# Performance work log

Measured on AMD Instinct MI355X. Metric: run time of the kernel, lower is better.

The kernel has to match this reference:

```python
import jax, jax.numpy as jnp
import numpy as np

N_NODES = 20000
N_EDGES = 320000
IN_CH = 256
HID = 128
HEADS = 4
OUT_CH = 200
NUM_GRAPHS = 64
NEG_SLOPE = 0.2


def setup_inputs() -> dict:
    key = jax.random.key(0)
    ks = jax.random.split(key, 16)
    x = jax.random.normal(ks[0], (N_NODES, IN_CH), dtype=jnp.float32)
    edge_index = jax.random.randint(ks[1], (2, N_EDGES), 0, N_NODES, dtype=jnp.int64)
    batch = jnp.sort(jax.random.randint(ks[2], (N_NODES,), 0, NUM_GRAPHS, dtype=jnp.int64))

    def lin(k, fan_in, fan_out):
        return jax.random.normal(k, (fan_in, fan_out), dtype=jnp.float32) / np.sqrt(fan_in)

    def att(k, h, c):
        return jax.random.normal(k, (h, c), dtype=jnp.float32) / np.sqrt(c)

    return {
        "x": x, "edge_index": edge_index, "batch": batch,
        "W1": lin(ks[3], IN_CH, HEADS * HID),
        "a_src1": att(ks[4], HEADS, HID), "a_dst1": att(ks[5], HEADS, HID),
        "b1": jnp.zeros((HEADS * HID,), jnp.float32),
        "W2": lin(ks[6], HEADS * HID, HEADS * HID),
        "a_src2": att(ks[7], HEADS, HID), "a_dst2": att(ks[8], HEADS, HID),
        "b2": jnp.zeros((HEADS * HID,), jnp.float32),
        "W3": lin(ks[9], HEADS * HID, HID),
        "a_src3": att(ks[10], 1, HID), "a_dst3": att(ks[11], 1, HID),
        "b3": jnp.zeros((HID,), jnp.float32),
        "fc_w": lin(ks[12], HID, OUT_CH),
        "fc_b": jnp.zeros((OUT_CH,), jnp.float32),
    }


def gat_conv(x, src, dst, W, a_src, a_dst, bias):
    """PyG GATConv (concat=True, negative_slope=0.2, self-loops appended by caller)."""
    N = x.shape[0]
    heads, out_ch = a_src.shape
    h = (x @ W).reshape(N, heads, out_ch)                 # [N,H,C]
    alpha_s = jnp.einsum('nhc,hc->nh', h, a_src)          # [N,H]
    alpha_d = jnp.einsum('nhc,hc->nh', h, a_dst)
    e = jax.nn.leaky_relu(alpha_s[src] + alpha_d[dst], NEG_SLOPE)  # [E,H]
    # segment softmax over edges sharing the same target node
    m = jax.ops.segment_max(e, dst, num_segments=N)
    e = jnp.exp(e - m[dst])
    denom = jax.ops.segment_sum(e, dst, num_segments=N)
    alpha = e / (denom[dst] + 1e-16)                      # [E,H]
    msg = h[src] * alpha[:, :, None]                      # [E,H,C]
    out = jax.ops.segment_sum(msg, dst, num_segments=N)   # [N,H,C]
    return out.reshape(N, heads * out_ch) + bias


def reference(x, edge_index, batch, W1, a_src1, a_dst1, b1,
              W2, a_src2, a_dst2, b2, W3, a_src3, a_dst3, b3, fc_w, fc_b):
    N = x.shape[0]
    loop = jnp.arange(N, dtype=edge_index.dtype)
    src = jnp.concatenate([edge_index[0], loop])
    dst = jnp.concatenate([edge_index[1], loop])

    h = jax.nn.elu(gat_conv(x, src, dst, W1, a_src1, a_dst1, b1))
    h = jax.nn.elu(gat_conv(h, src, dst, W2, a_src2, a_dst2, b2))
    h = jax.nn.elu(gat_conv(h, src, dst, W3, a_src3, a_dst3, b3))

    # global_mean_pool over graph ids
    sums = jax.ops.segment_sum(h, batch, num_segments=NUM_GRAPHS)
    cnts = jax.ops.segment_sum(jnp.ones((N,), h.dtype), batch, num_segments=NUM_GRAPHS)
    pooled = sums / jnp.maximum(cnts, 1.0)[:, None]       # [G,HID]
    # F.dropout with training=False is identity
    logits = pooled @ fc_w + fc_b                          # [G,OUT_CH]
    return logits
```

## Files before the change

kernel.cpp:

```cpp
#include <hip/hip_runtime.h>
#include <hip/hip_bf16.h>
#include <stdint.h>

#define N_NODES   20000
#define N_EDGES   320000
#define E_TOT     (N_EDGES + N_NODES)
#define IN_CH     256
#define HID       128
#define HEADS     4
#define OUT_CH    200
#define NUM_GRAPHS 64
#define M_PAD     20096

typedef __bf16 bf16_t;
typedef __bf16 bf16x8 __attribute__((ext_vector_type(8)));
typedef __bf16 bf16x2 __attribute__((ext_vector_type(2)));
typedef float  f32x4  __attribute__((ext_vector_type(4)));

__device__ __forceinline__ bool detect_bf16(const unsigned short* __restrict__ xu16) {
  int lane = threadIdx.x & 63;
  unsigned short v = xu16[2 * lane];
  int e = (v >> 7) & 0xff;
  unsigned long long b = __ballot(e >= 90 && e <= 160);
  return __popcll(b) >= 40;
}
__device__ __forceinline__ bool detect_i64(const unsigned* __restrict__ eidx) {
  int lane = threadIdx.x & 63;
  unsigned long long b = __ballot(eidx[2 * lane + 1] == 0u);
  return __popcll(b) >= 32;
}

struct SmallCvt {
  const void* src[11];
  bf16_t* dst[11];
  int n[11];
};

__global__ void prep(const void* __restrict__ W1, const void* __restrict__ W2,
                     const void* __restrict__ W3, bf16_t* __restrict__ W1T,
                     bf16_t* __restrict__ W2T, bf16_t* __restrict__ W3T,
                     SmallCvt tab, const unsigned short* __restrict__ xu16,
                     const int* __restrict__ eidx, const int* __restrict__ batch,
                     int* __restrict__ esrc, int* __restrict__ edst,
                     int* __restrict__ b32, int* __restrict__ deg) {
  bool isbf = detect_bf16(xu16);
  bool i64  = detect_i64((const unsigned*)eidx);
  int i = blockIdx.x * 256 + threadIdx.x;
  if (i < N_EDGES) {
    int s = i64 ? eidx[2 * i] : eidx[i];
    int d = i64 ? eidx[2 * (N_EDGES + i)] : eidx[N_EDGES + i];
    esrc[i] = s;
    edst[i] = d;
    atomicAdd(&deg[d], 1);
  }
  if (i < N_NODES) {
    b32[i] = i64 ? batch[2 * i] : batch[i];
    atomicAdd(&deg[i], 1);
  }
  if (i < 131072) {
    int k = i >> 9, nn = i & 511;
    bf16_t v = isbf ? ((const bf16_t*)W1)[i] : (bf16_t)((const float*)W1)[i];
    W1T[(size_t)nn * 256 + k] = v;
  } else if (i < 131072 + 262144) {
    int i2 = i - 131072;
    int k = i2 >> 9, nn = i2 & 511;
    bf16_t v = isbf ? ((const bf16_t*)W2)[i2] : (bf16_t)((const float*)W2)[i2];
    W2T[(size_t)nn * 512 + k] = v;
  } else if (i < 131072 + 262144 + 65536) {
    int i3 = i - 131072 - 262144;
    int k = i3 >> 7, nn = i3 & 127;
    bf16_t v = isbf ? ((const bf16_t*)W3)[i3] : (bf16_t)((const float*)W3)[i3];
    W3T[(size_t)nn * 512 + k] = v;
  } else {
    int j = i - 458752;
    for (int s = 0; s < 11; ++s) {
      if (j < tab.n[s]) {
        tab.dst[s][j] = isbf ? ((const bf16_t*)tab.src[s])[j]
                             : (bf16_t)((const float*)tab.src[s])[j];
        break;
      }
      j -= tab.n[s];
    }
  }
}

__launch_bounds__(1024)
__global__ void scan_deg_block(const int* __restrict__ deg, int* __restrict__ off,
                               int* __restrict__ cursor) {
  const int PT = 20;
  int t = threadIdx.x;
  int lane = t & 63, wid = t >> 6;
  int base = t * PT;
  int v[PT];
  int s = 0;
#pragma unroll
  for (int j = 0; j < PT; ++j) {
    int i = base + j;
    v[j] = (i < N_NODES) ? deg[i] : 0;
    s += v[j];
  }
  int x = s;
  for (int d = 1; d < 64; d <<= 1) {
    int y = __shfl_up(x, d);
    if (lane >= d) x += y;
  }
  __shared__ int wsum[16];
  if (lane == 63) wsum[wid] = x;
  __syncthreads();
  if (t < 16) {
    int y = wsum[t];
    for (int d = 1; d < 16; d <<= 1) {
      int z = __shfl_up(y, d);
      if (t >= d) y += z;
    }
    wsum[t] = y;
  }
  __syncthreads();
  int run = (wid > 0 ? wsum[wid - 1] : 0) + (x - s);
#pragma unroll
  for (int j = 0; j < PT; ++j) {
    int i = base + j;
    if (i < N_NODES) { off[i] = run; cursor[i] = 0; run += v[j]; }
  }
  if (t == 1023) off[N_NODES] = run;
}

__global__ void scatter_kernel(const int* __restrict__ esrc, const int* __restrict__ edst,
                               const int* __restrict__ off, int* __restrict__ cursor,
                               int* __restrict__ csr_src) {
  int e = blockIdx.x * 256 + threadIdx.x;
  if (e >= E_TOT) return;
  int s, d;
  if (e < N_EDGES) { s = esrc[e]; d = edst[e]; } else { s = d = e - N_EDGES; }
  int pos = off[d] + atomicAdd(&cursor[d], 1);
  csr_src[pos] = s;
}

template<bool MAYBE_F32, int NBN>
__launch_bounds__(256)
__global__ void gemm_bf16(const void* __restrict__ Av, const bf16_t* __restrict__ BT,
                          bf16_t* __restrict__ C, int M, int N, int K,
                          const bf16_t* __restrict__ a_src, const bf16_t* __restrict__ a_dst,
                          float* __restrict__ as, float* __restrict__ ad, int H) {
  bool isbf = MAYBE_F32 ? detect_bf16((const unsigned short*)Av) : true;
  const bf16_t* A  = (const bf16_t*)Av;
  const float*  Af = (const float*)Av;
  __shared__ bf16_t As[2][128 * 32];
  __shared__ bf16_t Bs[2][128 * 32];
  __shared__ float sred[2][128];
  __shared__ float dred[2][128];
  const int tid  = threadIdx.x;
  const int lane = tid & 63;
  const int w    = tid >> 6;
  const int wm   = w & 1, wn = w >> 1;
  const int id   = blockIdx.x;
  const int bmq  = id / (8 * NBN);
  const int rem  = id % (8 * NBN);
  const int bm   = (bmq * 8 + (rem & 7)) * 128;
  const int bn   = (rem >> 3) * 128;
  const int quad = lane >> 4;
  const int l16  = lane & 15;
  const int hd   = bn >> 7;

  f32x4 zero = {0.f, 0.f, 0.f, 0.f};
  f32x4 acc[4][4];
  for (int i = 0; i < 4; ++i)
    for (int j = 0; j < 4; ++j) acc[i][j] = zero;

  const int c0 = tid, c1 = tid + 256;
  const int r0 = c0 >> 2, s0 = c0 & 3;
  const int r1 = c1 >> 2, s1 = c1 & 3;
  int ga0 = bm + r0; if (ga0 > M - 1) ga0 = M - 1;
  int ga1 = bm + r1; if (ga1 > M - 1) ga1 = M - 1;

  auto stage = [&](int b, int k0) {
    __builtin_amdgcn_global_load_lds(
        (const __attribute__((address_space(1))) void*)(A + (size_t)ga0 * K + k0 + s0 * 8),
        (__attribute__((address_space(3))) void*)(&As[b][(size_t)(w * 64) * 8]), 16, 0, 0);
    __builtin_amdgcn_global_load_lds(
        (const __attribute__((address_space(1))) void*)(BT + (size_t)(bn + r0) * K + k0 + s0 * 8),
        (__attribute__((address_space(3))) void*)(&Bs[b][(size_t)(w * 64) * 8]), 16, 0, 0);
    __builtin_amdgcn_global_load_lds(
        (const __attribute__((address_space(1))) void*)(A + (size_t)ga1 * K + k0 + s1 * 8),
        (__attribute__((address_space(3))) void*)(&As[b][(size_t)(256 + w * 64) * 8]), 16, 0, 0);
    __builtin_amdgcn_global_load_lds(
        (const __attribute__((address_space(1))) void*)(BT + (size_t)(bn + r1) * K + k0 + s1 * 8),
        (__attribute__((address_space(3))) void*)(&Bs[b][(size_t)(256 + w * 64) * 8]), 16, 0, 0);
  };

  auto mma_step = [&](int b) {
    bf16x8 af[4], bfr[4];
    for (int mt = 0; mt < 4; ++mt) {
      int m_local = wm * 64 + mt * 16 + l16;
      af[mt] = *(const bf16x8*)(&As[b][m_local * 32 + quad * 8]);
    }
    for (int nt = 0; nt < 4; ++nt) {
      int n_local = wn * 64 + nt * 16 + l16;
      bfr[nt] = *(const bf16x8*)(&Bs[b][n_local * 32 + quad * 8]);
    }
    for (int mt = 0; mt < 4; ++mt)
      for (int nt = 0; nt < 4; ++nt)
        acc[mt][nt] = __builtin_amdgcn_mfma_f32_16x16x32_bf16(af[mt], bfr[nt], acc[mt][nt], 0, 0, 0);
  };

  if (!MAYBE_F32 || isbf) {
    stage(0, 0);
    __syncthreads();
    const int NT = K >> 5;
    for (int t = 0; t < NT; ++t) {
      int cur = t & 1;
      if (t + 1 < NT) stage(cur ^ 1, (t + 1) << 5);
      mma_step(cur);
      __syncthreads();
    }
  } else {
    for (int k0 = 0; k0 < K; k0 += 32) {
      bf16x8 va0, va1;
      const float* p0 = Af + (size_t)ga0 * K + k0 + s0 * 8;
      const float* p1 = Af + (size_t)ga1 * K + k0 + s1 * 8;
      f32x4 l0 = *(const f32x4*)p0, h0 = *(const f32x4*)(p0 + 4);
      f32x4 l1 = *(const f32x4*)p1, h1 = *(const f32x4*)(p1 + 4);
      for (int j = 0; j < 4; ++j) {
        va0[j] = (bf16_t)l0[j]; va0[j + 4] = (bf16_t)h0[j];
        va1[j] = (bf16_t)l1[j]; va1[j + 4] = (bf16_t)h1[j];
      }
      bf16x8 vb0 = *(const bf16x8*)(BT + (size_t)(bn + r0) * K + k0 + s0 * 8);
      bf16x8 vb1 = *(const bf16x8*)(BT + (size_t)(bn + r1) * K + k0 + s1 * 8);
      __syncthreads();
      *(bf16x8*)(&As[0][c0 * 8]) = va0;
      *(bf16x8*)(&Bs[0][c0 * 8]) = vb0;
      *(bf16x8*)(&As[0][c1 * 8]) = va1;
      *(bf16x8*)(&Bs[0][c1 * 8]) = vb1;
      __syncthreads();
      mma_step(0);
    }
  }

  for (int mt = 0; mt < 4; ++mt) {
    for (int r = 0; r < 4; ++r) {
      int m = bm + wm * 64 + mt * 16 + quad * 4 + r;
      if (m >= M) continue;
      for (int nt = 0; nt < 4; ++nt) {
        int n = bn + wn * 64 + nt * 16 + l16;
        C[(size_t)m * N + n] = (bf16_t)acc[mt][nt][r];
      }
    }
  }

  float av[4], dv[4];
  for (int nt = 0; nt < 4; ++nt) {
    int ch = wn * 64 + nt * 16 + l16;
    av[nt] = (float)a_src[hd * 128 + ch];
    dv[nt] = (float)a_dst[hd * 128 + ch];
  }
  for (int mt = 0; mt < 4; ++mt) {
    for (int r = 0; r < 4; ++r) {
      float s = acc[mt][0][r] * av[0] + acc[mt][1][r] * av[1]
              + acc[mt][2][r] * av[2] + acc[mt][3][r] * av[3];
      float d = acc[mt][0][r] * dv[0] + acc[mt][1][r] * dv[1]
              + acc[mt][2][r] * dv[2] + acc[mt][3][r] * dv[3];
      for (int o = 1; o < 16; o <<= 1) {
        s += __shfl_xor(s, o);
        d += __shfl_xor(d, o);
      }
      if (l16 == 0) {
        int row_local = wm * 64 + mt * 16 + quad * 4 + r;
        sred[wn][row_local] = s;
        dred[wn][row_local] = d;
      }
    }
  }
  __syncthreads();
  if (tid < 128) {
    int m = bm + tid;
    if (m < M) {
      as[m * H + hd] = sred[0][tid] + sred[1][tid];
      ad[m * H + hd] = dred[0][tid] + dred[1][tid];
    }
  }
}

template<int CPL>
__launch_bounds__(256)
__global__ void agg_fused(const bf16_t* __restrict__ h, const int* __restrict__ off,
                          const int* __restrict__ csr_src, const float* __restrict__ as,
                          const float* __restrict__ ad, const bf16_t* __restrict__ bias,
                          bf16_t* __restrict__ outp, int H) {
  typedef __bf16 vec_t __attribute__((ext_vector_type(CPL)));
  const int C = CPL * 64;
  int lane = threadIdx.x & 63;
  int n = blockIdx.x * 4 + (threadIdx.x >> 6);
  if (n >= N_NODES) return;
  int start = __builtin_amdgcn_readfirstlane(off[n]);
  int end   = __builtin_amdgcn_readfirstlane(off[n + 1]);
  int c0 = lane * CPL;
  int hd = c0 >> 7;
  float adv = ad[n * H + hd];
  float acc[CPL];
  for (int j = 0; j < CPL; ++j) acc[j] = 0.f;
  float den = 0.f;

  int pos = start;
  for (; pos + 3 < end; pos += 4) {
    int s0 = __builtin_amdgcn_readfirstlane(csr_src[pos]);
    int s1 = __builtin_amdgcn_readfirstlane(csr_src[pos + 1]);
    int s2 = __builtin_amdgcn_readfirstlane(csr_src[pos + 2]);
    int s3 = __builtin_amdgcn_readfirstlane(csr_src[pos + 3]);
    vec_t hv0 = *(const vec_t*)(h + (size_t)s0 * C + c0);
    vec_t hv1 = *(const vec_t*)(h + (size_t)s1 * C + c0);
    vec_t hv2 = *(const vec_t*)(h + (size_t)s2 * C + c0);
    vec_t hv3 = *(const vec_t*)(h + (size_t)s3 * C + c0);
    float e0 = as[s0 * H + hd] + adv; e0 = e0 > 0.f ? e0 : 0.2f * e0;
    float e1 = as[s1 * H + hd] + adv; e1 = e1 > 0.f ? e1 : 0.2f * e1;
    float e2 = as[s2 * H + hd] + adv; e2 = e2 > 0.f ? e2 : 0.2f * e2;
    float e3 = as[s3 * H + hd] + adv; e3 = e3 > 0.f ? e3 : 0.2f * e3;
    float w0 = __expf(e0), w1 = __expf(e1), w2 = __expf(e2), w3 = __expf(e3);
    den += (w0 + w1) + (w2 + w3);
    for (int j = 0; j < CPL; ++j)
      acc[j] += (w0 * (float)hv0[j] + w1 * (float)hv1[j])
              + (w2 * (float)hv2[j] + w3 * (float)hv3[j]);
  }
  for (; pos < end; ++pos) {
    int s0 = __builtin_amdgcn_readfirstlane(csr_src[pos]);
    vec_t hv0 = *(const vec_t*)(h + (size_t)s0 * C + c0);
    float e0 = as[s0 * H + hd] + adv; e0 = e0 > 0.f ? e0 : 0.2f * e0;
    float w0 = __expf(e0);
    den += w0;
    for (int j = 0; j < CPL; ++j) acc[j] += w0 * (float)hv0[j];
  }

  float inv = 1.f / (den + 1e-16f);
  vec_t ov;
  for (int j = 0; j < CPL; ++j) {
    float o = acc[j] * inv + (float)bias[c0 + j];
    o = o > 0.f ? o : expm1f(o);
    ov[j] = (bf16_t)o;
  }
  *(vec_t*)(outp + (size_t)n * C + c0) = ov;
}

__launch_bounds__(256)
__global__ void pool_fc2(const bf16_t* __restrict__ h3, const int* __restrict__ batch,
                         const bf16_t* __restrict__ fcw, const bf16_t* __restrict__ fcb,
                         void* __restrict__ outp, const unsigned short* __restrict__ xu16) {
  bool isbf = detect_bf16(xu16);
  int g = blockIdx.x;
  int lo = 0, hi = N_NODES;
  while (lo < hi) { int mid = (lo + hi) >> 1; if (batch[mid] < g) lo = mid + 1; else hi = mid; }
  int start = lo;
  hi = N_NODES;
  while (lo < hi) { int mid = (lo + hi) >> 1; if (batch[mid] < g + 1) lo = mid + 1; else hi = mid; }
  int end = lo, cnt = end - start;

  int t = threadIdx.x;
  int wave = t >> 6, lane = t & 63;
  int c0 = lane * 2;
  float a0 = 0.f, a1 = 0.f;
  for (int n = start + wave; n < end; n += 4) {
    bf16x2 v = *(const bf16x2*)(h3 + (size_t)n * HID + c0);
    a0 += (float)v[0];
    a1 += (float)v[1];
  }
  __shared__ float red[4][HID];
  red[wave][c0] = a0;
  red[wave][c0 + 1] = a1;
  __syncthreads();
  __shared__ float pooled[HID];
  if (t < HID) {
    float s = red[0][t] + red[1][t] + red[2][t] + red[3][t];
    pooled[t] = s / (float)(cnt > 0 ? cnt : 1);
  }
  __syncthreads();
  if (t < OUT_CH) {
    float a = (float)fcb[t];
    for (int c = 0; c < HID; ++c) a += pooled[c] * (float)fcw[c * OUT_CH + t];
    if (isbf) ((bf16_t*)outp)[g * OUT_CH + t] = (bf16_t)a;
    else      ((float*)outp)[g * OUT_CH + t] = a;
  }
}

extern "C" void kernel_launch(void* const* d_in, const int* in_sizes, int n_in,
                              void* d_out, int out_size, void* d_ws, size_t ws_size,
                              hipStream_t stream) {
  const void* x    = d_in[0];
  const void* eidx = d_in[1];
  const void* batch= d_in[2];
  const void* W1   = d_in[3];
  const void* a_s1 = d_in[4];
  const void* a_d1 = d_in[5];
  const void* b1   = d_in[6];
  const void* W2   = d_in[7];
  const void* a_s2 = d_in[8];
  const void* a_d2 = d_in[9];
  const void* b2   = d_in[10];
  const void* W3   = d_in[11];
  const void* a_s3 = d_in[12];
  const void* a_d3 = d_in[13];
  const void* b3   = d_in[14];
  const void* fcw  = d_in[15];
  const void* fcb  = d_in[16];
  const unsigned short* xu16 = (const unsigned short*)x;

  char* p = (char*)d_ws;
  auto carve = [&](size_t nbytes) { char* r = p; p += (nbytes + 255) & ~(size_t)255; return r; };
  bf16_t*   W1T    = (bf16_t*)carve((size_t)512 * 256 * 2);
  bf16_t*   W2T    = (bf16_t*)carve((size_t)512 * 512 * 2);
  bf16_t*   W3T    = (bf16_t*)carve((size_t)128 * 512 * 2);
  bf16_t*   hA     = (bf16_t*)carve((size_t)M_PAD * 512 * 2);
  bf16_t*   hB     = (bf16_t*)carve((size_t)M_PAD * 512 * 2);
  bf16_t*   sm     = (bf16_t*)carve((size_t)32768 * 2);
  bf16_t *as1b = sm, *ad1b = sm + 512, *b1b = sm + 1024,
         *as2b = sm + 1536, *ad2b = sm + 2048, *b2b = sm + 2560,
         *as3b = sm + 3072, *ad3b = sm + 3200, *b3b = sm + 3328,
         *fcwb = sm + 3456, *fcbb = sm + 29056;
  float*    asb    = (float*)carve((size_t)N_NODES * 4 * 4);
  float*    adb    = (float*)carve((size_t)N_NODES * 4 * 4);
  int*      deg    = (int*)carve((size_t)N_NODES * 4);
  int*      off    = (int*)carve((size_t)(N_NODES + 1) * 4);
  int*      cursor = (int*)carve((size_t)N_NODES * 4);
  int*      csr_src= (int*)carve((size_t)E_TOT * 4);
  int*      esrc32 = (int*)carve((size_t)N_EDGES * 4);
  int*      edst32 = (int*)carve((size_t)N_EDGES * 4);
  int*      bat32  = (int*)carve((size_t)N_NODES * 4);

  dim3 b256(256);
  const int NG4 = (N_NODES + 3) / 4;

  SmallCvt tab;
  const void* srcs[11] = {a_s1, a_d1, b1, a_s2, a_d2, b2, a_s3, a_d3, b3, fcw, fcb};
  bf16_t* dsts[11] = {as1b, ad1b, b1b, as2b, ad2b, b2b, as3b, ad3b, b3b, fcwb, fcbb};
  int ns[11] = {512, 512, 512, 512, 512, 512, 128, 128, 128, 25600, 200};
  for (int i = 0; i < 11; ++i) { tab.src[i] = srcs[i]; tab.dst[i] = dsts[i]; tab.n[i] = ns[i]; }

  hipMemsetAsync(deg, 0, (size_t)N_NODES * 4, stream);
  prep<<<dim3((458752 + 29256 + 255) / 256), b256, 0, stream>>>(
      W1, W2, W3, W1T, W2T, W3T, tab, xu16,
      (const int*)eidx, (const int*)batch, esrc32, edst32, bat32, deg);

  scan_deg_block<<<dim3(1), dim3(1024), 0, stream>>>(deg, off, cursor);
  scatter_kernel<<<dim3((E_TOT + 255) / 256), b256, 0, stream>>>(esrc32, edst32, off, cursor, csr_src);

  const int G4 = 160 * 4, G1 = 160 * 1;

  gemm_bf16<true, 4><<<dim3(G4), b256, 0, stream>>>(x, W1T, hA, N_NODES, 512, 256,
                                                    as1b, ad1b, asb, adb, 4);
  agg_fused<8><<<dim3(NG4), b256, 0, stream>>>(hA, off, csr_src, asb, adb, b1b, hB, 4);

  gemm_bf16<false, 4><<<dim3(G4), b256, 0, stream>>>(hB, W2T, hA, N_NODES, 512, 512,
                                                     as2b, ad2b, asb, adb, 4);
  agg_fused<8><<<dim3(NG4), b256, 0, stream>>>(hA, off, csr_src, asb, adb, b2b, hB, 4);

  gemm_bf16<false, 1><<<dim3(G1), b256, 0, stream>>>(hB, W3T, hA, N_NODES, 128, 512,
                                                     as3b, ad3b, asb, adb, 1);
  agg_fused<2><<<dim3(NG4), b256, 0, stream>>>(hA, off, csr_src, asb, adb, b3b, hB, 1);

  pool_fc2<<<dim3(NUM_GRAPHS), b256, 0, stream>>>(hB, bat32, fcwb, fcbb, d_out, xu16);
}
```

Baseline: 362.3 us.

## Split 4-head aggregation into edge-weight pass and XCD-sliced channel aggregation

For the two 4-head GAT layers, the fused aggregation is replaced by two passes over head pairs. A new kernel computes unnormalised exp attention weights per edge and per-node denominators into a scratch buffer that reuses the now-dead CSR build memory. A second kernel aggregates one 64-channel slice per wave, with block ids mapped so each XCD handles a fixed channel slice, so the gathered h columns stay resident in that XCD's L2. This trades extra launches and a write/read of edge weights for better cache locality on the random source-row gathers. Max subtraction is dropped from the softmax, which risks overflow for large logits.

```diff
diff --git a/kernel.cpp b/kernel.cpp
--- a/kernel.cpp
+++ b/kernel.cpp
@@ -280,6 +280,79 @@
   }
 }
 
+__launch_bounds__(256)
+__global__ void edge_w(const int* __restrict__ off, const int* __restrict__ csr_src,
+                       const float* __restrict__ as, const float* __restrict__ ad,
+                       float* __restrict__ wbuf, float* __restrict__ den, int h0) {
+  int lane = threadIdx.x & 63;
+  int n = blockIdx.x * 4 + (threadIdx.x >> 6);
+  if (n >= N_NODES) return;
+  int start = __builtin_amdgcn_readfirstlane(off[n]);
+  int end   = __builtin_amdgcn_readfirstlane(off[n + 1]);
+  int ei = lane >> 1, hh = h0 + (lane & 1);
+  float adv = ad[n * 4 + hh];
+  float psum = 0.f;
+  for (int p0 = start; p0 < end; p0 += 32) {
+    int p = p0 + ei;
+    bool valid = p < end;
+    int src = csr_src[valid ? p : end - 1];
+    float e = as[src * 4 + hh] + adv;
+    e = e > 0.f ? e : 0.2f * e;
+    float wv = __expf(e);
+    if (valid) {
+      __builtin_nontemporal_store(wv, &wbuf[(size_t)(lane & 1) * E_TOT + p]);
+      psum += wv;
+    }
+  }
+  for (int o = 2; o < 64; o <<= 1) psum += __shfl_xor(psum, o);
+  if (lane < 2) den[n * 4 + h0 + lane] = psum;
+}
+
+__launch_bounds__(256)
+__global__ void agg_sliced(const bf16_t* __restrict__ h, const int* __restrict__ off,
+                           const int* __restrict__ csr_src, const float* __restrict__ wbuf,
+                           const float* __restrict__ den, const bf16_t* __restrict__ bias,
+                           bf16_t* __restrict__ outp, int ch0) {
+  int lane  = threadIdx.x & 63;
+  int bid   = blockIdx.x;
+  int xcd   = bid & 7;
+  int slice = xcd >> 1;
+  int grp   = (bid >> 3) * 2 + (xcd & 1);
+  int n     = grp * 4 + (threadIdx.x >> 6);
+  if (n >= N_NODES) return;
+  int ch = ch0 + slice * 64 + lane;
+  int hd = ch >> 7;
+  int start = __builtin_amdgcn_readfirstlane(off[n]);
+  int end   = __builtin_amdgcn_readfirstlane(off[n + 1]);
+  const float* wp = wbuf + (size_t)(hd & 1) * E_TOT;
+  float acc = 0.f;
+  int pos = start;
+  for (; pos + 3 < end; pos += 4) {
+    int s0 = __builtin_amdgcn_readfirstlane(csr_src[pos]);
+    int s1 = __builtin_amdgcn_readfirstlane(csr_src[pos + 1]);
+    int s2 = __builtin_amdgcn_readfirstlane(csr_src[pos + 2]);
+    int s3 = __builtin_amdgcn_readfirstlane(csr_src[pos + 3]);
+    float w0 = __builtin_nontemporal_load(&wp[pos]);
+    float w1 = __builtin_nontemporal_load(&wp[pos + 1]);
+    float w2 = __builtin_nontemporal_load(&wp[pos + 2]);
+    float w3 = __builtin_nontemporal_load(&wp[pos + 3]);
+    float v0 = (float)h[(size_t)s0 * 512 + ch];
+    float v1 = (float)h[(size_t)s1 * 512 + ch];
+    float v2 = (float)h[(size_t)s2 * 512 + ch];
+    float v3 = (float)h[(size_t)s3 * 512 + ch];
+    acc += (w0 * v0 + w1 * v1) + (w2 * v2 + w3 * v3);
+  }
+  for (; pos < end; ++pos) {
+    int s0 = __builtin_amdgcn_readfirstlane(csr_src[pos]);
+    float w0 = __builtin_nontemporal_load(&wp[pos]);
+    acc += w0 * (float)h[(size_t)s0 * 512 + ch];
+  }
+  float dn = den[n * 4 + hd];
+  float o = acc / (dn + 1e-16f) + (float)bias[ch];
+  o = o > 0.f ? o : expm1f(o);
+  __builtin_nontemporal_store((bf16_t)o, &outp[(size_t)n * 512 + ch]);
+}
+
 template<int CPL>
 __launch_bounds__(256)
 __global__ void agg_fused(const bf16_t* __restrict__ h, const int* __restrict__ off,
@@ -415,13 +488,16 @@
          *fcwb = sm + 3456, *fcbb = sm + 29056;
   float*    asb    = (float*)carve((size_t)N_NODES * 4 * 4);
   float*    adb    = (float*)carve((size_t)N_NODES * 4 * 4);
-  int*      deg    = (int*)carve((size_t)N_NODES * 4);
+  float*    denb   = (float*)carve((size_t)N_NODES * 4 * 4);
   int*      off    = (int*)carve((size_t)(N_NODES + 1) * 4);
-  int*      cursor = (int*)carve((size_t)N_NODES * 4);
   int*      csr_src= (int*)carve((size_t)E_TOT * 4);
-  int*      esrc32 = (int*)carve((size_t)N_EDGES * 4);
-  int*      edst32 = (int*)carve((size_t)N_EDGES * 4);
   int*      bat32  = (int*)carve((size_t)N_NODES * 4);
+  char*     ov     = carve(2720256);
+  int*      deg    = (int*)ov;
+  int*      cursor = (int*)(ov + 80128);
+  int*      esrc32 = (int*)(ov + 160256);
+  int*      edst32 = (int*)(ov + 1440256);
+  float*    wbuf   = (float*)ov;
 
   dim3 b256(256);
   const int NG4 = (N_NODES + 3) / 4;
@@ -441,14 +517,21 @@
   scatter_kernel<<<dim3((E_TOT + 255) / 256), b256, 0, stream>>>(esrc32, edst32, off, cursor, csr_src);
 
   const int G4 = 160 * 4, G1 = 160 * 1;
+  const int NSL = (NG4 / 2) * 8;
 
   gemm_bf16<true, 4><<<dim3(G4), b256, 0, stream>>>(x, W1T, hA, N_NODES, 512, 256,
                                                     as1b, ad1b, asb, adb, 4);
-  agg_fused<8><<<dim3(NG4), b256, 0, stream>>>(hA, off, csr_src, asb, adb, b1b, hB, 4);
+  edge_w<<<dim3(NG4), b256, 0, stream>>>(off, csr_src, asb, adb, wbuf, denb, 0);
+  agg_sliced<<<dim3(NSL), b256, 0, stream>>>(hA, off, csr_src, wbuf, denb, b1b, hB, 0);
+  edge_w<<<dim3(NG4), b256, 0, stream>>>(off, csr_src, asb, adb, wbuf, denb, 2);
+  agg_sliced<<<dim3(NSL), b256, 0, stream>>>(hA, off, csr_src, wbuf, denb, b1b, hB, 256);
 
   gemm_bf16<false, 4><<<dim3(G4), b256, 0, stream>>>(hB, W2T, hA, N_NODES, 512, 512,
                                                      as2b, ad2b, asb, adb, 4);
-  agg_fused<8><<<dim3(NG4), b256, 0, stream>>>(hA, off, csr_src, asb, adb, b2b, hB, 4);
+  edge_w<<<dim3(NG4), b256, 0, stream>>>(off, csr_src, asb, adb, wbuf, denb, 0);
+  agg_sliced<<<dim3(NSL), b256, 0, stream>>>(hA, off, csr_src, wbuf, denb, b2b, hB, 0);
+  edge_w<<<dim3(NG4), b256, 0, stream>>>(off, csr_src, asb, adb, wbuf, denb, 2);
+  agg_sliced<<<dim3(NSL), b256, 0, stream>>>(hA, off, csr_src, wbuf, denb, b2b, hB, 256);
 
   gemm_bf16<false, 1><<<dim3(G1), b256, 0, stream>>>(hB, W3T, hA, N_NODES, 128, 512,
                                                      as3b, ad3b, asb, adb, 1);
```

After: 487.8 us. +34.7%, slower.
